# Performance work log

Hardware: AMD Instinct MI355X
Metric: run time of the kernel (lower is better)

## Reference

```python
import jax, jax.numpy as jnp
import numpy as np

B, T, D_IN, D_H = 4, 8192, 512, 512


def log_g(x):
    # log of g(x) = where(x>=0, x+0.5, sigmoid(x))
    return jnp.where(x >= 0, jnp.log(jax.nn.relu(x) + 0.5), -jax.nn.softplus(-x))


def setup_inputs() -> dict:
    key = jax.random.key(0)
    ks = jax.random.split(key, 8)
    s = 1.0 / np.sqrt(D_IN)
    return {
        "x": jax.random.normal(ks[0], (B, T, D_IN), jnp.float32),
        "h_0": jax.random.uniform(ks[1], (B, 1, D_H), jnp.float32),
        "Wf": jax.random.uniform(ks[2], (D_H, D_IN), jnp.float32, -s, s),
        "bf": jax.random.uniform(ks[3], (D_H,), jnp.float32, -s, s),
        "Wi": jax.random.uniform(ks[4], (D_H, D_IN), jnp.float32, -s, s),
        "bi": jax.random.uniform(ks[5], (D_H,), jnp.float32, -s, s),
        "Wh": jax.random.uniform(ks[6], (D_H, D_IN), jnp.float32, -s, s),
        "bh": jax.random.uniform(ks[7], (D_H,), jnp.float32, -s, s),
    }


def reference(x, h_0, Wf, bf, Wi, bi, Wh, bh):
    # projections: (B, T, D_H)
    f_pre = jnp.einsum("bti,hi->bth", x, Wf) + bf
    i_pre = jnp.einsum("bti,hi->bth", x, Wi) + bi
    h_pre = jnp.einsum("bti,hi->bth", x, Wh) + bh

    diff = jax.nn.softplus(-f_pre) - jax.nn.softplus(-i_pre)
    log_f = -jax.nn.softplus(diff)   # log sigma-normalized forget gate
    log_i = -jax.nn.softplus(-diff)  # log input gate

    log_h0 = log_g(h_0)              # (B, 1, D_H)
    log_tilde_h = log_g(h_pre)       # (B, T, D_H)
    log_values = jnp.concatenate([log_h0, log_i + log_tilde_h], axis=1)  # (B, T+1, D_H)

    # parallel_scan_log: h_t = exp(a*_t + logcumsumexp(values - a*))
    a_star = jnp.pad(jnp.cumsum(log_f, axis=1), ((0, 0), (1, 0), (0, 0)))  # (B, T+1, D_H)
    log_h = a_star + jax.lax.cumlogsumexp(log_values - a_star, axis=1)
    return jnp.exp(log_h)[:, 1:]  # (B, T, D_H)
```

## Files before the change

kernel.cpp:

```cpp
#include <hip/hip_runtime.h>
#include <hip/hip_bf16.h>
#include <stdint.h>

#define T_SEQ 8192
#define BB    4
#define DH    512
#define DIN   512
#define M_TOT (BB*T_SEQ)
#define BM    128
#define BCH   64
#define BK    64
#define NKT   24
#define KS    1024
#define CHUNK_L 128
#define NCHUNK  64
#define NCH_TOT (BB*DH)
#define GRID_WG 2048
#define LDS_HALF 20480

#define XB_BLOCKS 8192
#define BM_BLOCKS 384

typedef __attribute__((ext_vector_type(4))) float f32x4;
typedef __attribute__((ext_vector_type(8))) short bf16x8;

__device__ __forceinline__ unsigned short f2bf_rne(float x){
  unsigned u = __float_as_uint(x);
  return (unsigned short)((u + 0x7FFFu + ((u >> 16) & 1u)) >> 16);
}
__device__ __forceinline__ float bf2f(unsigned short h){
  return __uint_as_float(((unsigned)h) << 16);
}
__device__ __forceinline__ void gld16(const void* g, void* l){
  __builtin_amdgcn_global_load_lds((const __attribute__((address_space(1))) unsigned*)g,
                                   (__attribute__((address_space(3))) unsigned*)l, 16, 0, 0);
}

__device__ __forceinline__ void split8_store(const float* src, unsigned short* dhi){
  float4 a = *(const float4*)src;
  float4 b = *(const float4*)(src + 4);
  float xs[8] = {a.x, a.y, a.z, a.w, b.x, b.y, b.z, b.w};
  unsigned short hi[8], lo[8];
#pragma unroll
  for (int e = 0; e < 8; ++e){
    hi[e] = f2bf_rne(xs[e]);
    lo[e] = f2bf_rne(xs[e] - bf2f(hi[e]));
  }
  uint4 ph, pl;
  ph.x = hi[0] | ((unsigned)hi[1] << 16); ph.y = hi[2] | ((unsigned)hi[3] << 16);
  ph.z = hi[4] | ((unsigned)hi[5] << 16); ph.w = hi[6] | ((unsigned)hi[7] << 16);
  pl.x = lo[0] | ((unsigned)lo[1] << 16); pl.y = lo[2] | ((unsigned)lo[3] << 16);
  pl.z = lo[4] | ((unsigned)lo[5] << 16); pl.w = lo[6] | ((unsigned)lo[7] << 16);
  *(uint4*)dhi = ph;
  *(uint4*)(dhi + 512) = pl;
}

__global__ void aug_build(const float* __restrict__ X,
                          const float* __restrict__ Wf, const float* __restrict__ Wi,
                          const float* __restrict__ Wh,
                          unsigned short* __restrict__ Xa, unsigned short* __restrict__ Bm,
                          int with_xa){
  int bx = blockIdx.x;
  if (with_xa && bx < XB_BLOCKS){
    int g = bx * 256 + threadIdx.x;
    int row  = g >> 6;
    int tile = (g >> 3) & 7;
    int clog = g & 7;
    int cphys = clog ^ (row & 7);
    split8_store(X + (size_t)row * DIN + tile * 64 + clog * 8,
                 Xa + (size_t)row * KS + tile * 64 + cphys * 8);
  } else {
    int g = (bx - (with_xa ? XB_BLOCKS : 0)) * 256 + threadIdx.x;
    int gate = g >> 15;
    int ch   = (g >> 6) & 511;
    int tile = (g >> 3) & 7;
    int clog = g & 7;
    const float* W = (gate == 0) ? Wf : ((gate == 1) ? Wi : Wh);
    int cphys = clog ^ (ch & 7);
    split8_store(W + (size_t)ch * DIN + tile * 64 + clog * 8,
                 Bm + (size_t)(gate * 512 + ch) * KS + tile * 64 + cphys * 8);
  }
}

__device__ __forceinline__ void gate_epilogue3(const f32x4 acc[4][3], int m0, int c0,
                                               int wm, int wn, int lr, int lg,
                                               const float* bfb, const float* bib, const float* bhb,
                                               float* Fw, float* Vw){
  int chan = c0 + wn * 16 + lr;
  float bfv = bfb[chan], biv = bib[chan], bhv = bhb[chan];
#pragma unroll
  for (int mi = 0; mi < 4; ++mi){
#pragma unroll
    for (int r = 0; r < 4; ++r){
      int bt = m0 + wm * 64 + mi * 16 + lg * 4 + r;
      float fp = acc[mi][0][r] + bfv;
      float ip = acc[mi][1][r] + biv;
      float hp = acc[mi][2][r] + bhv;
      float zf = -fp, zi = -ip;
      float spf = fmaxf(zf, 0.f) + log1pf(expf(-fabsf(zf)));
      float spi = fmaxf(zi, 0.f) + log1pf(expf(-fabsf(zi)));
      float ef  = expf(spf - spi);
      float fg  = 1.f / (1.f + ef);
      float g   = (hp >= 0.f) ? (hp + 0.5f) : (1.f / (1.f + expf(-hp)));
      float v   = (1.f - fg) * g;
      size_t idx = (size_t)bt * DH + chan;
      Fw[idx] = fg;
      Vw[idx] = v;
    }
  }
}

__launch_bounds__(512, 4)
__global__ void gemm_fast(const unsigned short* __restrict__ Xa, const unsigned short* __restrict__ Bm,
                          const float* __restrict__ bfb, const float* __restrict__ bib,
                          const float* __restrict__ bhb,
                          float* __restrict__ Fw, float* __restrict__ Vw){
  __shared__ unsigned short smem[2 * LDS_HALF];
  const int tid = threadIdx.x, wid = tid >> 6, lane = tid & 63;
  const int wg = (blockIdx.x & 7) * (GRID_WG / 8) + (blockIdx.x >> 3);
  const int m0 = (wg >> 3) * BM, c0 = (wg & 7) * BCH;
  const int wm = wid >> 2, wn = wid & 3, lr = lane & 15, lg = lane >> 4;

  const unsigned short* aS0 = Xa + (size_t)(m0 + (tid >> 3)) * KS + (tid & 7) * 8;
  const unsigned short* aS1 = aS0 + (size_t)64 * KS;
  const unsigned short* bS[3];
#pragma unroll
  for (int q = 0; q < 3; ++q){
    int ci = q * 512 + tid, row = ci >> 3, cp = ci & 7;
    bS[q] = Bm + (size_t)((row >> 6) * 512 + c0 + (row & 63)) * KS + cp * 8;
  }
  const int ldst = (tid & ~63) * 8;

  f32x4 acc[4][3];
#pragma unroll
  for (int a = 0; a < 4; ++a)
#pragma unroll
    for (int b = 0; b < 3; ++b) acc[a][b] = {0.f, 0.f, 0.f, 0.f};

  auto stage = [&](int kt, unsigned short* buf){
    const int aoff = (kt < 16 ? kt : kt - 16) * 64;
    const int boff = (kt < 8  ? kt : kt - 8 ) * 64;
    unsigned short* aD = buf + ldst;
    gld16(aS0 + aoff, aD);
    gld16(aS1 + aoff, aD + 4096);
    unsigned short* bD = buf + 8192 + ldst;
#pragma unroll
    for (int q = 0; q < 3; ++q) gld16(bS[q] + boff, bD + q * 4096);
  };

  stage(0, smem);
  __syncthreads();
  int cur = 0;
  for (int kt = 0; kt < NKT; ++kt){
    if (kt + 1 < NKT) stage(kt + 1, smem + (cur ^ 1) * LDS_HALF);
    unsigned short* lA = smem + cur * LDS_HALF;
    unsigned short* lB = lA + 8192;
#pragma unroll
    for (int kk = 0; kk < 2; ++kk){
      bf16x8 af[4], bfr[3];
#pragma unroll
      for (int mi = 0; mi < 4; ++mi){
        int row = wm * 64 + mi * 16 + lr;
        int ch  = (kk * 4 + lg) ^ (row & 7);
        af[mi] = *(const bf16x8*)(lA + row * 64 + ch * 8);
      }
#pragma unroll
      for (int j = 0; j < 3; ++j){
        int row = j * 64 + wn * 16 + lr;
        int ch  = (kk * 4 + lg) ^ (row & 7);
        bfr[j] = *(const bf16x8*)(lB + row * 64 + ch * 8);
      }
#pragma unroll
      for (int mi = 0; mi < 4; ++mi)
#pragma unroll
        for (int j = 0; j < 3; ++j)
          acc[mi][j] = __builtin_amdgcn_mfma_f32_16x16x32_bf16(af[mi], bfr[j], acc[mi][j], 0, 0, 0);
    }
    __syncthreads();
    cur ^= 1;
  }
  gate_epilogue3(acc, m0, c0, wm, wn, lr, lg, bfb, bib, bhb, Fw, Vw);
}

__launch_bounds__(512, 2)
__global__ void gemm_slow(const float* __restrict__ X, const unsigned short* __restrict__ Bm,
                          const float* __restrict__ bfb, const float* __restrict__ bib,
                          const float* __restrict__ bhb,
                          float* __restrict__ Fw, float* __restrict__ Vw){
  __shared__ unsigned short smem[LDS_HALF];
  unsigned short* lA = smem;
  unsigned short* lB = smem + 8192;
  const int tid = threadIdx.x, wid = tid >> 6, lane = tid & 63;
  const int m0 = blockIdx.x * BM, c0 = blockIdx.y * BCH;
  const int wm = wid >> 2, wn = wid & 3, lr = lane & 15, lg = lane >> 4;

  const unsigned short* bS[3];
#pragma unroll
  for (int q = 0; q < 3; ++q){
    int ci = q * 512 + tid, row = ci >> 3, cp = ci & 7;
    bS[q] = Bm + (size_t)((row >> 6) * 512 + c0 + (row & 63)) * KS + cp * 8;
  }
  unsigned short* bD0 = lB + (size_t)(tid & ~63) * 8;

  f32x4 acc[4][3];
#pragma unroll
  for (int a = 0; a < 4; ++a)
#pragma unroll
    for (int b = 0; b < 3; ++b) acc[a][b] = {0.f, 0.f, 0.f, 0.f};

  for (int kt = 0; kt < NKT; ++kt){
    const bool losec = (kt >= 8 && kt < 16);
    const int  ko    = (kt < 8 ? kt : (kt < 16 ? kt - 8 : kt - 16)) * 64;
    const int  boff  = (kt < 8 ? kt : kt - 8) * 64;
    if (kt) __syncthreads();
#pragma unroll
    for (int q = 0; q < 2; ++q){
      int ci = q * 512 + tid, row = ci >> 3, kc = ci & 7;
      const float* src = X + (size_t)(m0 + row) * DIN + ko + kc * 8;
      float4 xa = *(const float4*)src;
      float4 xb = *(const float4*)(src + 4);
      float xs[8] = {xa.x, xa.y, xa.z, xa.w, xb.x, xb.y, xb.z, xb.w};
      unsigned short hs[8];
#pragma unroll
      for (int e = 0; e < 8; ++e){
        unsigned short h = f2bf_rne(xs[e]);
        hs[e] = losec ? f2bf_rne(xs[e] - bf2f(h)) : h;
      }
      uint4 pk;
      pk.x = hs[0] | ((unsigned)hs[1] << 16); pk.y = hs[2] | ((unsigned)hs[3] << 16);
      pk.z = hs[4] | ((unsigned)hs[5] << 16); pk.w = hs[6] | ((unsigned)hs[7] << 16);
      *(uint4*)(lA + row * 64 + ((kc ^ (row & 7)) * 8)) = pk;
    }
#pragma unroll
    for (int q = 0; q < 3; ++q) gld16(bS[q] + boff, bD0 + q * 4096);
    __syncthreads();
#pragma unroll
    for (int kk = 0; kk < 2; ++kk){
      bf16x8 af[4], bfr[3];
#pragma unroll
      for (int mi = 0; mi < 4; ++mi){
        int row = wm * 64 + mi * 16 + lr;
        int ch  = (kk * 4 + lg) ^ (row & 7);
        af[mi] = *(const bf16x8*)(lA + row * 64 + ch * 8);
      }
#pragma unroll
      for (int j = 0; j < 3; ++j){
        int row = j * 64 + wn * 16 + lr;
        int ch  = (kk * 4 + lg) ^ (row & 7);
        bfr[j] = *(const bf16x8*)(lB + row * 64 + ch * 8);
      }
#pragma unroll
      for (int mi = 0; mi < 4; ++mi)
#pragma unroll
        for (int j = 0; j < 3; ++j)
          acc[mi][j] = __builtin_amdgcn_mfma_f32_16x16x32_bf16(af[mi], bfr[j], acc[mi][j], 0, 0, 0);
    }
  }
  gate_epilogue3(acc, m0, c0, wm, wn, lr, lg, bfb, bib, bhb, Fw, Vw);
}

__global__ void scan_chunks(const float* __restrict__ Fw, const float* __restrict__ Vw,
                            float2* __restrict__ S){
  int bx = blockIdx.x;
  int chunk = bx >> 2, b = bx & 3;
  int ch4 = threadIdx.x * 4;
  size_t base = ((size_t)(b * T_SEQ + chunk * CHUNK_L)) * DH + ch4;
  float4 Fc = make_float4(1.f, 1.f, 1.f, 1.f);
  float4 Vc = make_float4(0.f, 0.f, 0.f, 0.f);
#pragma unroll 8
  for (int t = 0; t < CHUNK_L; ++t){
    float4 f = *(const float4*)(Fw + base + (size_t)t * DH);
    float4 v = *(const float4*)(Vw + base + (size_t)t * DH);
    Fc.x *= f.x; Fc.y *= f.y; Fc.z *= f.z; Fc.w *= f.w;
    Vc.x = fmaf(f.x, Vc.x, v.x); Vc.y = fmaf(f.y, Vc.y, v.y);
    Vc.z = fmaf(f.z, Vc.z, v.z); Vc.w = fmaf(f.w, Vc.w, v.w);
  }
  float2* s = S + (size_t)chunk * NCH_TOT + b * DH + ch4;
  s[0] = make_float2(Fc.x, Vc.x);
  s[1] = make_float2(Fc.y, Vc.y);
  s[2] = make_float2(Fc.z, Vc.z);
  s[3] = make_float2(Fc.w, Vc.w);
}

__global__ void scan_carry(const float2* __restrict__ S, const float* __restrict__ h0,
                           float* __restrict__ Hs){
  int cg = blockIdx.x * 256 + threadIdx.x;
  float hv = h0[cg];
  float h = (hv >= 0.f) ? (hv + 0.5f) : (1.f / (1.f + expf(-hv)));
  float2 s = S[cg];
#pragma unroll 16
  for (int k = 0; k < NCHUNK; ++k){
    float2 snext = (k + 1 < NCHUNK) ? S[(k + 1) * NCH_TOT + cg] : make_float2(0.f, 0.f);
    Hs[k * NCH_TOT + cg] = h;
    h = fmaf(s.x, h, s.y);
    s = snext;
  }
}

__global__ void scan_apply(const float* __restrict__ Fw, const float* Vw,
                           const float* __restrict__ Hs, float* out){
  int bx = blockIdx.x;
  int chunk = bx >> 2, b = bx & 3;
  int ch4 = threadIdx.x * 4;
  float4 h = *(const float4*)(Hs + (size_t)chunk * NCH_TOT + b * DH + ch4);
  size_t base = ((size_t)(b * T_SEQ + chunk * CHUNK_L)) * DH + ch4;
#pragma unroll 8
  for (int t = 0; t < CHUNK_L; ++t){
    size_t idx = base + (size_t)t * DH;
    float4 f = *(const float4*)(Fw + idx);
    float4 v = *(const float4*)(Vw + idx);
    h.x = fmaf(f.x, h.x, v.x); h.y = fmaf(f.y, h.y, v.y);
    h.z = fmaf(f.z, h.z, v.z); h.w = fmaf(f.w, h.w, v.w);
    *(float4*)(out + idx) = h;
  }
}

extern "C" void kernel_launch(void* const* d_in, const int* in_sizes, int n_in,
                              void* d_out, int out_size, void* d_ws, size_t ws_size,
                              hipStream_t stream){
  (void)in_sizes; (void)n_in; (void)out_size;
  const float* X  = (const float*)d_in[0];
  const float* h0 = (const float*)d_in[1];
  const float* Wf = (const float*)d_in[2];
  const float* bf = (const float*)d_in[3];
  const float* Wi = (const float*)d_in[4];
  const float* bi = (const float*)d_in[5];
  const float* Wh = (const float*)d_in[6];
  const float* bh = (const float*)d_in[7];

  constexpr size_t XA_B = (size_t)M_TOT * KS * 2;
  constexpr size_t F_B  = (size_t)M_TOT * DH * 4;
  constexpr size_t S_B  = (size_t)NCHUNK * NCH_TOT * 8;
  constexpr size_t H_B  = (size_t)NCHUNK * NCH_TOT * 4;
  constexpr size_t BMB  = (size_t)3 * 512 * KS * 2;
  const bool fast = ws_size >= XA_B + F_B + S_B + H_B + BMB;

  char* ws = (char*)d_ws;
  float* Vw  = (float*)d_out;
  float* out = (float*)d_out;

  if (fast){
    unsigned short* Xa  = (unsigned short*)ws;
    float*          Fw  = (float*)(ws + XA_B);
    float2*         S   = (float2*)(ws + XA_B + F_B);
    float*          Hs  = (float*)(ws + XA_B + F_B + S_B);
    unsigned short* Bmw = (unsigned short*)(ws + XA_B + F_B + S_B + H_B);
    aug_build <<<XB_BLOCKS + BM_BLOCKS, 256, 0, stream>>>(X, Wf, Wi, Wh, Xa, Bmw, 1);
    gemm_fast <<<GRID_WG, 512, 0, stream>>>(Xa, Bmw, bf, bi, bh, Fw, Vw);
    scan_chunks<<<256, 128, 0, stream>>>(Fw, Vw, S);
    scan_carry <<<8, 256, 0, stream>>>(S, h0, Hs);
    scan_apply <<<256, 128, 0, stream>>>(Fw, Vw, Hs, out);
  } else {
    float*          Fw  = (float*)ws;
    float2*         S   = (float2*)(ws + F_B);
    float*          Hs  = (float*)(ws + F_B + S_B);
    unsigned short* Bmw = (unsigned short*)(ws + F_B + S_B + H_B);
    aug_build <<<BM_BLOCKS, 256, 0, stream>>>(X, Wf, Wi, Wh, nullptr, Bmw, 0);
    gemm_slow <<<dim3(M_TOT / BM, DH / BCH), 512, 0, stream>>>(X, Bmw, bf, bi, bh, Fw, Vw);
    scan_chunks<<<256, 128, 0, stream>>>(Fw, Vw, S);
    scan_carry <<<8, 256, 0, stream>>>(S, h0, Hs);
    scan_apply <<<256, 128, 0, stream>>>(Fw, Vw, Hs, out);
  }
}
```

Baseline: 449.5 us.

## Fuse chunk-summary scan into GEMM epilogue and unroll double-buffer loop

The GEMM epilogue now composes the per-row (forget, value) affine pairs into a per-chunk summary for each channel through shared-memory reduction stages and writes it to S directly. This removes the separate scan_chunks kernel, which had to re-read Fw and Vw from global memory. The K loop is also unrolled into explicit ping-pong buffers, and the MFMA block is wrapped in s_setprio to favour matrix issue. The cost is extra LDS work and two extra barriers in the GEMM tail.

```diff
diff --git a/kernel.cpp b/kernel.cpp
--- a/kernel.cpp
+++ b/kernel.cpp
@@ -82,6 +82,16 @@
   }
 }
 
+__device__ __forceinline__ void gates_eval(float fp, float ip, float hp, float& fg, float& v){
+  float zf = -fp, zi = -ip;
+  float spf = fmaxf(zf, 0.f) + log1pf(expf(-fabsf(zf)));
+  float spi = fmaxf(zi, 0.f) + log1pf(expf(-fabsf(zi)));
+  float ef  = expf(spf - spi);
+  fg = 1.f / (1.f + ef);
+  float g = (hp >= 0.f) ? (hp + 0.5f) : (1.f / (1.f + expf(-hp)));
+  v = (1.f - fg) * g;
+}
+
 __device__ __forceinline__ void gate_epilogue3(const f32x4 acc[4][3], int m0, int c0,
                                                int wm, int wn, int lr, int lg,
                                                const float* bfb, const float* bib, const float* bhb,
@@ -93,16 +103,8 @@
 #pragma unroll
     for (int r = 0; r < 4; ++r){
       int bt = m0 + wm * 64 + mi * 16 + lg * 4 + r;
-      float fp = acc[mi][0][r] + bfv;
-      float ip = acc[mi][1][r] + biv;
-      float hp = acc[mi][2][r] + bhv;
-      float zf = -fp, zi = -ip;
-      float spf = fmaxf(zf, 0.f) + log1pf(expf(-fabsf(zf)));
-      float spi = fmaxf(zi, 0.f) + log1pf(expf(-fabsf(zi)));
-      float ef  = expf(spf - spi);
-      float fg  = 1.f / (1.f + ef);
-      float g   = (hp >= 0.f) ? (hp + 0.5f) : (1.f / (1.f + expf(-hp)));
-      float v   = (1.f - fg) * g;
+      float fg, v;
+      gates_eval(acc[mi][0][r] + bfv, acc[mi][1][r] + biv, acc[mi][2][r] + bhv, fg, v);
       size_t idx = (size_t)bt * DH + chan;
       Fw[idx] = fg;
       Vw[idx] = v;
@@ -114,7 +116,8 @@
 __global__ void gemm_fast(const unsigned short* __restrict__ Xa, const unsigned short* __restrict__ Bm,
                           const float* __restrict__ bfb, const float* __restrict__ bib,
                           const float* __restrict__ bhb,
-                          float* __restrict__ Fw, float* __restrict__ Vw){
+                          float* __restrict__ Fw, float* __restrict__ Vw,
+                          float2* __restrict__ S){
   __shared__ unsigned short smem[2 * LDS_HALF];
   const int tid = threadIdx.x, wid = tid >> 6, lane = tid & 63;
   const int wg = (blockIdx.x & 7) * (GRID_WG / 8) + (blockIdx.x >> 3);
@@ -130,6 +133,8 @@
     bS[q] = Bm + (size_t)((row >> 6) * 512 + c0 + (row & 63)) * KS + cp * 8;
   }
   const int ldst = (tid & ~63) * 8;
+  unsigned short* buf0 = smem;
+  unsigned short* buf1 = smem + LDS_HALF;
 
   f32x4 acc[4][3];
 #pragma unroll
@@ -148,13 +153,8 @@
     for (int q = 0; q < 3; ++q) gld16(bS[q] + boff, bD + q * 4096);
   };
 
-  stage(0, smem);
-  __syncthreads();
-  int cur = 0;
-  for (int kt = 0; kt < NKT; ++kt){
-    if (kt + 1 < NKT) stage(kt + 1, smem + (cur ^ 1) * LDS_HALF);
-    unsigned short* lA = smem + cur * LDS_HALF;
-    unsigned short* lB = lA + 8192;
+  auto compute = [&](const unsigned short* lA){
+    const unsigned short* lB = lA + 8192;
 #pragma unroll
     for (int kk = 0; kk < 2; ++kk){
       bf16x8 af[4], bfr[3];
@@ -170,16 +170,75 @@
         int ch  = (kk * 4 + lg) ^ (row & 7);
         bfr[j] = *(const bf16x8*)(lB + row * 64 + ch * 8);
       }
+      __builtin_amdgcn_s_setprio(1);
 #pragma unroll
       for (int mi = 0; mi < 4; ++mi)
 #pragma unroll
         for (int j = 0; j < 3; ++j)
           acc[mi][j] = __builtin_amdgcn_mfma_f32_16x16x32_bf16(af[mi], bfr[j], acc[mi][j], 0, 0, 0);
-    }
+      __builtin_amdgcn_s_setprio(0);
+    }
+  };
+
+  stage(0, buf0);
+  __syncthreads();
+  for (int it = 0; it < NKT / 2; ++it){
+    stage(2 * it + 1, buf1);
+    compute(buf0);
     __syncthreads();
-    cur ^= 1;
-  }
-  gate_epilogue3(acc, m0, c0, wm, wn, lr, lg, bfb, bib, bhb, Fw, Vw);
+    if (2 * it + 2 < NKT) stage(2 * it + 2, buf0);
+    compute(buf1);
+    __syncthreads();
+  }
+
+  float2* pairs = (float2*)smem;
+  float2* part4 = ((float2*)smem) + 64 * 32;
+  const int chan_l = wn * 16 + lr;
+  const int chan   = c0 + chan_l;
+  {
+    float bfv = bfb[chan], biv = bib[chan], bhv = bhb[chan];
+#pragma unroll
+    for (int mi = 0; mi < 4; ++mi){
+      float F4 = 1.f, V4 = 0.f;
+#pragma unroll
+      for (int r = 0; r < 4; ++r){
+        int bt = m0 + wm * 64 + mi * 16 + lg * 4 + r;
+        float fg, v;
+        gates_eval(acc[mi][0][r] + bfv, acc[mi][1][r] + biv, acc[mi][2][r] + bhv, fg, v);
+        size_t idx = (size_t)bt * DH + chan;
+        Fw[idx] = fg;
+        Vw[idx] = v;
+        F4 = fg * F4;
+        V4 = fmaf(fg, V4, v);
+      }
+      pairs[chan_l * 32 + wm * 16 + mi * 4 + lg] = make_float2(F4, V4);
+    }
+  }
+  __syncthreads();
+  if (tid < 256){
+    int cl = tid >> 2, q = tid & 3;
+    float F = 1.f, V = 0.f;
+#pragma unroll
+    for (int i = 0; i < 8; ++i){
+      float2 pr = pairs[cl * 32 + q * 8 + i];
+      F = pr.x * F;
+      V = fmaf(pr.x, V, pr.y);
+    }
+    part4[cl * 4 + q] = make_float2(F, V);
+  }
+  __syncthreads();
+  if (tid < 64){
+    float F = 1.f, V = 0.f;
+#pragma unroll
+    for (int i = 0; i < 4; ++i){
+      float2 pr = part4[tid * 4 + i];
+      F = pr.x * F;
+      V = fmaf(pr.x, V, pr.y);
+    }
+    int b     = m0 >> 13;
+    int chunk = (m0 & 8191) >> 7;
+    S[chunk * NCH_TOT + b * DH + c0 + tid] = make_float2(F, V);
+  }
 }
 
 __launch_bounds__(512, 2)
@@ -346,8 +405,7 @@
     float*          Hs  = (float*)(ws + XA_B + F_B + S_B);
     unsigned short* Bmw = (unsigned short*)(ws + XA_B + F_B + S_B + H_B);
     aug_build <<<XB_BLOCKS + BM_BLOCKS, 256, 0, stream>>>(X, Wf, Wi, Wh, Xa, Bmw, 1);
-    gemm_fast <<<GRID_WG, 512, 0, stream>>>(Xa, Bmw, bf, bi, bh, Fw, Vw);
-    scan_chunks<<<256, 128, 0, stream>>>(Fw, Vw, S);
+    gemm_fast <<<GRID_WG, 512, 0, stream>>>(Xa, Bmw, bf, bi, bh, Fw, Vw, S);
     scan_carry <<<8, 256, 0, stream>>>(S, h0, Hs);
     scan_apply <<<256, 128, 0, stream>>>(Fw, Vw, Hs, out);
   } else {
```

New measurement: 411.3 us. 8.5% less time.
